# Kernel optimization log

Hardware: AMD Instinct MI355X
Metric: run time of the kernel (lower is better)

Reference implementation:

```python
import jax, jax.numpy as jnp
import numpy as np

B, S, D, H = 4, 2048, 1024, 4
HD = D // H


def setup_inputs() -> dict:
    key = jax.random.key(0)
    ks = jax.random.split(key, 6)
    s = 0.02  # init scale for projection weights
    return {
        "hidden_states": jax.random.normal(ks[0], (B, S, D), jnp.float32),
        "Wq": jax.random.normal(ks[1], (D, D), jnp.float32) * s,
        "Wk": jax.random.normal(ks[2], (D, D), jnp.float32) * s,
        "Wv": jax.random.normal(ks[3], (D, D), jnp.float32) * s,
        "Wo": jax.random.normal(ks[4], (D, D), jnp.float32) * s,
        "bo": jnp.zeros((D,), jnp.float32),
        "betas": jax.random.normal(ks[5], (1, H, 1, 1), jnp.float32),
        "mem": jnp.zeros((H, HD, HD), jnp.float32),
        "z": jnp.zeros((H, HD, 1), jnp.float32),
    }


def reference(hidden_states, Wq, Wk, Wv, Wo, bo, betas, mem, z):
    b, s, d = hidden_states.shape
    h = betas.shape[1]
    hd = d // h

    def split(x):  # [b,s,d] -> [b,h,s,hd]
        return x.reshape(b, s, h, hd).transpose(0, 2, 1, 3)

    q = split(hidden_states @ Wq.T)
    k = split(hidden_states @ Wk.T)
    v = split(hidden_states @ Wv.T)

    # standard causal attention (note: no 1/sqrt(d) scaling, faithful to source)
    aw = jnp.einsum('bhqd,bhkd->bhqk', q, k)
    causal = jnp.tril(jnp.ones((s, s), bool))
    aw = jnp.where(causal, aw, jnp.finfo(aw.dtype).min)
    p = jax.nn.softmax(aw, axis=-1)
    attn = jnp.einsum('bhqk,bhkd->bhqd', p, v)

    # linear-attention memory read
    sq = jax.nn.elu(q) + 1.0
    sk = jax.nn.elu(k) + 1.0
    A_mem = jnp.einsum('bhsd,hde->bhse', sq, mem) / (
        jnp.einsum('bhsd,hdo->bhso', sq, z) + 1e-6)

    # sigmoid-gated blend
    g = jax.nn.sigmoid(betas)
    out = g * A_mem + (1.0 - g) * attn

    # memory / z state update (delta rule), averaged over batch
    delta = jnp.einsum('bhsd,hde->bhse', sk, mem) / (
        jnp.einsum('bhsd,hdo->bhso', sk, z) + 1e-6)
    mem_new = mem + jnp.einsum('bhsd,bhse->hde', sk, v - delta) / b
    z_new = z + jnp.mean(jnp.sum(sk, axis=2), axis=0)[:, :, None]

    # merge heads + output projection
    out = out.transpose(0, 2, 1, 3).reshape(b, s, d)
    out = out @ Wo.T + bo
    return (out, mem_new, z_new)
```

## Files before the change

kernel.cpp:

```cpp
#include <hip/hip_runtime.h>

#define Bsz 4
#define Ssz 2048
#define Dsz 1024
#define Hsz 4
#define HDsz 256
#define Msz 8192

typedef unsigned short u16;
typedef __attribute__((ext_vector_type(8))) short bf16x8;
typedef __attribute__((ext_vector_type(4))) float f32x4;

__device__ __forceinline__ u16 f2b(float f) {
  unsigned u = __float_as_uint(f);
  return (u16)((u + 0x7FFFu + ((u >> 16) & 1u)) >> 16);
}
__device__ __forceinline__ unsigned pk2(float a, float b) {
  return (unsigned)f2b(a) | ((unsigned)f2b(b) << 16);
}

typedef const unsigned int __attribute__((address_space(1)))* gcp;
typedef unsigned int __attribute__((address_space(3)))* lcp;
__device__ __forceinline__ void gld16(const u16* g, u16* l) {
  __builtin_amdgcn_global_load_lds((gcp)g, (lcp)l, 16, 0, 0);
}

__global__ __launch_bounds__(256) void cvt_bf16(const float4* __restrict__ in,
                                                u16* __restrict__ outp) {
  size_t i = (size_t)blockIdx.x * 256 + threadIdx.x;
  float4 v = in[i];
  uint2 r; r.x = pk2(v.x, v.y); r.y = pk2(v.z, v.w);
  *(uint2*)(outp + i * 4) = r;
}

__global__ __launch_bounds__(256) void gemm_lds(const u16* __restrict__ A16,
                                                const u16* __restrict__ Wb,
                                                const float* __restrict__ bias,
                                                float* __restrict__ C32,
                                                u16* __restrict__ Cbf) {
  __shared__ u16 sA[128 * 32];
  __shared__ u16 sB[128 * 32];
  const int tid = threadIdx.x;
  const int lane = tid & 63, quad = lane >> 4, l15 = lane & 15;
  const int w = tid >> 6;
  const int mw = (w >> 1) * 64, nw = (w & 1) * 64;
  const int m0 = blockIdx.y * 128, n0 = blockIdx.x * 128;
  const int r0 = tid >> 2, seg = (tid & 3) * 8;
  const u16* ga0 = A16 + (size_t)(m0 + r0) * Dsz + seg;
  const u16* gb0 = Wb + (size_t)(n0 + r0) * Dsz + seg;
  u16* lA0 = sA + w * 512;
  u16* lA1 = sA + 2048 + w * 512;
  u16* lB0 = sB + w * 512;
  u16* lB1 = sB + 2048 + w * 512;
  f32x4 acc[4][4] = {};
  for (int k0 = 0; k0 < Dsz; k0 += 32) {
    __syncthreads();
    gld16(ga0 + k0, lA0);
    gld16(ga0 + (size_t)64 * Dsz + k0, lA1);
    gld16(gb0 + k0, lB0);
    gld16(gb0 + (size_t)64 * Dsz + k0, lB1);
    __syncthreads();
    bf16x8 af[4], bfr[4];
#pragma unroll
    for (int i = 0; i < 4; ++i) {
      af[i] = *(const bf16x8*)&sA[(mw + i * 16 + l15) * 32 + quad * 8];
      bfr[i] = *(const bf16x8*)&sB[(nw + i * 16 + l15) * 32 + quad * 8];
    }
#pragma unroll
    for (int i = 0; i < 4; ++i)
#pragma unroll
      for (int j = 0; j < 4; ++j)
        acc[i][j] = __builtin_amdgcn_mfma_f32_16x16x32_bf16(af[i], bfr[j], acc[i][j], 0, 0, 0);
  }
#pragma unroll
  for (int j = 0; j < 4; ++j) {
    const int n = n0 + nw + j * 16 + l15;
    const float bv = bias ? bias[n] : 0.f;
#pragma unroll
    for (int i = 0; i < 4; ++i) {
#pragma unroll
      for (int r = 0; r < 4; ++r) {
        const int m = m0 + mw + i * 16 + quad * 4 + r;
        const float val = acc[i][j][r] + bv;
        const size_t idx = (size_t)m * Dsz + n;
        if (C32) C32[idx] = val;
        if (Cbf) Cbf[idx] = f2b(val);
      }
    }
  }
}

__global__ __launch_bounds__(256) void transpose_v(const float* __restrict__ V,
                                                   u16* __restrict__ Vt) {
  __shared__ u16 tile[32 * 36];
  const int t = threadIdx.x;
  const int s0 = blockIdx.x * 32, e0 = blockIdx.y * 32, bh = blockIdx.z;
  const int b = bh >> 2, h = bh & 3;
  {
    const int s_l = t >> 3, e8 = (t & 7) * 4;
    float4 v = *(const float4*)(V + ((size_t)(b * Ssz) + s0 + s_l) * Dsz + h * HDsz + e0 + e8);
    uint2 r; r.x = pk2(v.x, v.y); r.y = pk2(v.z, v.w);
    *(uint2*)&tile[s_l * 36 + e8] = r;
  }
  __syncthreads();
  {
    const int e_l = t >> 3, s4 = (t & 7) * 4;
    u16 a = tile[(s4 + 0) * 36 + e_l], b2 = tile[(s4 + 1) * 36 + e_l];
    u16 c = tile[(s4 + 2) * 36 + e_l], d = tile[(s4 + 3) * 36 + e_l];
    uint2 r; r.x = (unsigned)a | ((unsigned)b2 << 16);
    r.y = (unsigned)c | ((unsigned)d << 16);
    *(uint2*)(Vt + ((size_t)bh * HDsz + e0 + e_l) * Ssz + s0 + s4) = r;
  }
}

__global__ __launch_bounds__(256) void attn_mfma(const u16* __restrict__ Qg,
                                                 const u16* __restrict__ Kg,
                                                 const u16* __restrict__ Vtg,
                                                 float* __restrict__ At,
                                                 float* __restrict__ Pb,
                                                 float* __restrict__ mlb) {
  static const unsigned char tab[52] = {
      (unsigned char)(31|0x80), (unsigned char)(31|0xC0),
      (unsigned char)(30|0x80), (unsigned char)(30|0xC0),
      (unsigned char)(29|0x80), (unsigned char)(29|0xC0),
      (unsigned char)(28|0x80), (unsigned char)(28|0xC0),
      (unsigned char)(27|0x80), (unsigned char)(27|0xC0),
      (unsigned char)(26|0x80), (unsigned char)(26|0xC0),
      (unsigned char)(25|0x80), (unsigned char)(25|0xC0),
      (unsigned char)(24|0x80), (unsigned char)(24|0xC0),
      (unsigned char)(23|0x80), (unsigned char)(23|0xC0),
      11,
      (unsigned char)(22|0x80), (unsigned char)(22|0xC0),
      (unsigned char)(21|0x80), (unsigned char)(21|0xC0),
      10,
      (unsigned char)(20|0x80), (unsigned char)(20|0xC0),
      (unsigned char)(19|0x80), (unsigned char)(19|0xC0),
      9,
      (unsigned char)(18|0x80), (unsigned char)(18|0xC0),
      (unsigned char)(17|0x80), (unsigned char)(17|0xC0),
      8,
      (unsigned char)(16|0x80), (unsigned char)(16|0xC0),
      (unsigned char)(15|0x80), (unsigned char)(15|0xC0),
      7,
      (unsigned char)(14|0x80), (unsigned char)(14|0xC0),
      (unsigned char)(13|0x80), (unsigned char)(13|0xC0),
      6,
      (unsigned char)(12|0x80), (unsigned char)(12|0xC0),
      5, 4, 3, 2, 1, 0};
  const int e = tab[blockIdx.x];
  const int qt = e & 63, cc = (e >> 6) & 1;
  const bool split = (e >> 7) != 0;
  const int bh = blockIdx.y, b = bh >> 2, h = bh & 3;
  const int tid = threadIdx.x, w = tid >> 6, lane = tid & 63;
  const int quad = lane >> 4, l15 = lane & 15;
  __shared__ u16 sK[2][32 * 256];
  __shared__ u16 sV[2][256 * 32];
  const int q0w = qt * 64 + w * 16;
  bf16x8 qf[8];
  {
    const u16* qp = Qg + ((size_t)(b * Ssz) + q0w + l15) * Dsz + h * HDsz + quad * 8;
#pragma unroll
    for (int dd = 0; dd < 8; ++dd) qf[dd] = *(const bf16x8*)(qp + dd * 32);
  }
  f32x4 o[16] = {};
  float m_old = -1e30f, l = 0.f;
  const int nkt = 2 * qt + 2, half = qt + 1;
  const int kt_lo = (split && cc) ? half : 0;
  const int kt_hi = (split && !cc) ? half : nkt;
  const u16* kstage = Kg + ((size_t)(b * Ssz) + (tid >> 5)) * Dsz + h * HDsz
                      + (((tid & 31) ^ ((tid >> 5) & 7)) << 3);
  const u16* vstage = Vtg + ((size_t)bh * HDsz + (tid >> 2)) * Ssz
                      + (((tid & 3) ^ ((tid >> 3) & 3)) << 3);
  int bufc = 0;
  {
    const u16* kp = kstage + (size_t)(kt_lo * 32) * Dsz;
    const u16* vp = vstage + kt_lo * 32;
#pragma unroll
    for (int i = 0; i < 4; ++i) {
      gld16(kp + (size_t)i * 8 * Dsz, &sK[0][w * 512 + i * 2048]);
      gld16(vp + (size_t)i * 64 * Ssz, &sV[0][w * 512 + i * 2048]);
    }
  }
  for (int kt = kt_lo; kt < kt_hi; ++kt) {
    const int j0 = kt * 32;
    __syncthreads();
    if (kt + 1 < kt_hi) {
      const u16* kp = kstage + (size_t)((kt + 1) * 32) * Dsz;
      const u16* vp = vstage + (kt + 1) * 32;
      const int bn = bufc ^ 1;
#pragma unroll
      for (int i = 0; i < 4; ++i) {
        gld16(kp + (size_t)i * 8 * Dsz, &sK[bn][w * 512 + i * 2048]);
        gld16(vp + (size_t)i * 64 * Ssz, &sV[bn][w * 512 + i * 2048]);
      }
    }
    f32x4 s0v = {}, s1v = {};
    __builtin_amdgcn_s_setprio(1);
#pragma unroll
    for (int dd = 0; dd < 8; ++dd) {
      const int c0 = ((dd * 4 + quad) ^ (l15 & 7)) << 3;
      bf16x8 a0 = *(const bf16x8*)&sK[bufc][l15 * 256 + c0];
      bf16x8 a1 = *(const bf16x8*)&sK[bufc][(16 + l15) * 256 + c0];
      s0v = __builtin_amdgcn_mfma_f32_16x16x32_bf16(a0, qf[dd], s0v, 0, 0, 0);
      s1v = __builtin_amdgcn_mfma_f32_16x16x32_bf16(a1, qf[dd], s1v, 0, 0, 0);
    }
    __builtin_amdgcn_s_setprio(0);
    const int qg = q0w + l15;
    float p[8];
#pragma unroll
    for (int r = 0; r < 4; ++r) {
      const int kg = j0 + quad * 4 + r;
      p[r] = (kg <= qg) ? s0v[r] : -1e30f;
      p[4 + r] = (kg + 16 <= qg) ? s1v[r] : -1e30f;
    }
    float mt = p[0];
#pragma unroll
    for (int i = 1; i < 8; ++i) mt = fmaxf(mt, p[i]);
    mt = fmaxf(mt, __shfl_xor(mt, 16));
    mt = fmaxf(mt, __shfl_xor(mt, 32));
    const float m_new = fmaxf(m_old, mt);
    const float alpha = __expf(m_old - m_new);
    float ts = 0.f;
#pragma unroll
    for (int i = 0; i < 8; ++i) { p[i] = __expf(p[i] - m_new); ts += p[i]; }
    ts += __shfl_xor(ts, 16);
    ts += __shfl_xor(ts, 32);
    l = l * alpha + ts;
    m_old = m_new;
    if (!__all(alpha == 1.0f)) {
      const float a0_ = __shfl(alpha, (lane & 48) | (quad * 4 + 0));
      const float a1_ = __shfl(alpha, (lane & 48) | (quad * 4 + 1));
      const float a2_ = __shfl(alpha, (lane & 48) | (quad * 4 + 2));
      const float a3_ = __shfl(alpha, (lane & 48) | (quad * 4 + 3));
#pragma unroll
      for (int ds = 0; ds < 16; ++ds) {
        o[ds][0] *= a0_; o[ds][1] *= a1_; o[ds][2] *= a2_; o[ds][3] *= a3_;
      }
    }
    float xx[8];
#pragma unroll
    for (int i = 0; i < 8; ++i) xx[i] = __shfl_xor(p[i], 16);
    const bool qe = (quad & 1) == 0;
    float Alo[8], Ahi[8];
#pragma unroll
    for (int i = 0; i < 4; ++i) {
      Alo[i] = qe ? p[i] : xx[i];
      Alo[4 + i] = qe ? xx[i] : p[i];
      Ahi[i] = qe ? p[4 + i] : xx[4 + i];
      Ahi[4 + i] = qe ? xx[4 + i] : p[4 + i];
    }
    float zz[8];
    const bool sendlo = (quad & 1) != 0;
#pragma unroll
    for (int i = 0; i < 8; ++i) zz[i] = __shfl_xor(sendlo ? Alo[i] : Ahi[i], 32);
    float fin[8];
#pragma unroll
    for (int i = 0; i < 8; ++i)
      fin[i] = (quad == 0) ? Alo[i] : (quad == 3) ? Ahi[i] : zz[i];
    uint4 pkv;
    pkv.x = pk2(fin[0], fin[1]); pkv.y = pk2(fin[2], fin[3]);
    pkv.z = pk2(fin[4], fin[5]); pkv.w = pk2(fin[6], fin[7]);
    bf16x8 pf = *(bf16x8*)&pkv;
    const int vc0 = (quad ^ ((l15 >> 1) & 3)) << 3;
    __builtin_amdgcn_s_setprio(1);
#pragma unroll
    for (int ds = 0; ds < 16; ++ds) {
      bf16x8 bv = *(const bf16x8*)&sV[bufc][(ds * 16 + l15) * 32 + vc0];
      o[ds] = __builtin_amdgcn_mfma_f32_16x16x32_bf16(pf, bv, o[ds], 0, 0, 0);
    }
    __builtin_amdgcn_s_setprio(0);
    bufc ^= 1;
  }
  if (!split) {
    float lr[4];
#pragma unroll
    for (int r = 0; r < 4; ++r) lr[r] = 1.f / __shfl(l, (lane & 48) | (quad * 4 + r));
    float* ob = At + ((size_t)bh * Ssz + q0w + quad * 4) * HDsz + l15;
#pragma unroll
    for (int r = 0; r < 4; ++r)
#pragma unroll
      for (int ds = 0; ds < 16; ++ds)
        ob[(size_t)r * HDsz + ds * 16] = o[ds][r] * lr[r];
  } else {
    float* dst;
    if (cc == 0)
      dst = At + ((size_t)bh * Ssz + q0w + quad * 4) * HDsz + l15;
    else
      dst = Pb + ((size_t)((bh * 20 + (qt - 12)) * 64) + w * 16 + quad * 4) * HDsz + l15;
#pragma unroll
    for (int r = 0; r < 4; ++r)
#pragma unroll
      for (int ds = 0; ds < 16; ++ds)
        dst[(size_t)r * HDsz + ds * 16] = o[ds][r];
    if (lane < 16) {
      const int idx = (bh * 20 + (qt - 12)) * 64 + w * 16 + l15;
      mlb[cc * 40960 + idx] = m_old;
      mlb[cc * 40960 + 20480 + idx] = l;
    }
  }
}

__global__ __launch_bounds__(256) void attn_merge(float* __restrict__ At,
                                                  const float* __restrict__ Pb,
                                                  const float* __restrict__ mlb) {
  const int qx = blockIdx.x, bh = blockIdx.y;
  const int t = threadIdx.x;
  const int slot = (bh * 20 + qx) * 64;
  float4* abase = (float4*)(At + ((size_t)bh * Ssz + (12 + qx) * 64) * HDsz);
  const float4* pbase = (const float4*)(Pb + (size_t)slot * HDsz);
#pragma unroll
  for (int i = 0; i < 16; ++i) {
    const int f = i * 256 + t;
    const int qr = f >> 6;
    const int idx = slot + qr;
    const float m0 = mlb[idx], l0 = mlb[20480 + idx];
    const float m1 = mlb[40960 + idx], l1 = mlb[61440 + idx];
    const float mm = fmaxf(m0, m1);
    const float w0 = __expf(m0 - mm), w1 = __expf(m1 - mm);
    const float inv = 1.f / (l0 * w0 + l1 * w1);
    float4 av = abase[f];
    float4 pv = pbase[f];
    float4 ov;
    ov.x = (av.x * w0 + pv.x * w1) * inv;
    ov.y = (av.y * w0 + pv.y * w1) * inv;
    ov.z = (av.z * w0 + pv.z * w1) * inv;
    ov.w = (av.w * w0 + pv.w * w1) * inv;
    abase[f] = ov;
  }
}

__global__ __launch_bounds__(256) void eludens(float* __restrict__ Qb,
                                               float* __restrict__ Kb,
                                               const float* __restrict__ z,
                                               float* __restrict__ dq,
                                               float* __restrict__ dk) {
  const int wid = threadIdx.x >> 6, lane = threadIdx.x & 63;
  const int r = blockIdx.x * 4 + wid;
  const int b = r >> 13, h = (r >> 11) & 3, s = r & 2047;
  const size_t base = ((size_t)(b * Ssz + s)) * Dsz + h * HDsz + lane * 4;
  float4 z4 = *(const float4*)(z + h * HDsz + lane * 4);
  float4 q = *(float4*)(Qb + base);
  q.x = q.x > 0.f ? q.x + 1.f : __expf(q.x);
  q.y = q.y > 0.f ? q.y + 1.f : __expf(q.y);
  q.z = q.z > 0.f ? q.z + 1.f : __expf(q.z);
  q.w = q.w > 0.f ? q.w + 1.f : __expf(q.w);
  *(float4*)(Qb + base) = q;
  float4 k = *(float4*)(Kb + base);
  k.x = k.x > 0.f ? k.x + 1.f : __expf(k.x);
  k.y = k.y > 0.f ? k.y + 1.f : __expf(k.y);
  k.z = k.z > 0.f ? k.z + 1.f : __expf(k.z);
  k.w = k.w > 0.f ? k.w + 1.f : __expf(k.w);
  *(float4*)(Kb + base) = k;
  float pq = q.x * z4.x + q.y * z4.y + q.z * z4.z + q.w * z4.w;
  float pk = k.x * z4.x + k.y * z4.y + k.z * z4.z + k.w * z4.w;
#pragma unroll
  for (int off = 32; off; off >>= 1) {
    pq += __shfl_down(pq, off);
    pk += __shfl_down(pk, off);
  }
  if (lane == 0) { dq[r] = pq; dk[r] = pk; }
}

__global__ __launch_bounds__(256) void memread_mfma(const float* __restrict__ Asrc,
                                                    const float* __restrict__ mem,
                                                    const float* __restrict__ dens,
                                                    const float* __restrict__ betas,
                                                    const float* __restrict__ At,
                                                    float* __restrict__ Vio,
                                                    u16* __restrict__ bfout, int mode) {
  const int h = blockIdx.z;
  const int tid = threadIdx.x, lane = tid & 63, w = tid >> 6;
  const int quad = lane >> 4, l15 = lane & 15;
  const int mw = (w >> 1) * 64, ew = (w & 1) * 64;
  const int m0 = blockIdx.y * 128, e0t = blockIdx.x * 128;
  __shared__ u16 sA[128 * 40];
  __shared__ u16 sB[128 * 40];
  const int srow = tid >> 1, sseg = (tid & 1) * 16;
  const int k4 = (tid & 7) * 4, e4 = (tid >> 3) * 4;
  f32x4 acc[4][4] = {};
  for (int k0 = 0; k0 < HDsz; k0 += 32) {
    __syncthreads();
    {
      const float* ap = Asrc + (size_t)(m0 + srow) * Dsz + h * HDsz + k0 + sseg;
      float4 f0 = *(const float4*)ap, f1 = *(const float4*)(ap + 4);
      float4 f2 = *(const float4*)(ap + 8), f3 = *(const float4*)(ap + 12);
      uint4 u0, u1;
      u0.x = pk2(f0.x, f0.y); u0.y = pk2(f0.z, f0.w);
      u0.z = pk2(f1.x, f1.y); u0.w = pk2(f1.z, f1.w);
      u1.x = pk2(f2.x, f2.y); u1.y = pk2(f2.z, f2.w);
      u1.z = pk2(f3.x, f3.y); u1.w = pk2(f3.z, f3.w);
      u16* dst = &sA[srow * 40 + sseg];
      *(uint4*)dst = u0; *(uint4*)(dst + 8) = u1;
    }
    {
      const float* bp = mem + (size_t)h * 65536 + (size_t)(k0 + k4) * HDsz + e0t + e4;
      float4 r0 = *(const float4*)bp;
      float4 r1 = *(const float4*)(bp + HDsz);
      float4 r2 = *(const float4*)(bp + 2 * HDsz);
      float4 r3 = *(const float4*)(bp + 3 * HDsz);
      const float* rr[4] = {(const float*)&r0, (const float*)&r1,
                            (const float*)&r2, (const float*)&r3};
#pragma unroll
      for (int c = 0; c < 4; ++c) {
        uint2 u;
        u.x = pk2(rr[0][c], rr[1][c]);
        u.y = pk2(rr[2][c], rr[3][c]);
        *(uint2*)&sB[(e4 + c) * 40 + k4] = u;
      }
    }
    __syncthreads();
    bf16x8 af[4], bfr[4];
#pragma unroll
    for (int i = 0; i < 4; ++i) {
      af[i] = *(const bf16x8*)&sA[(mw + i * 16 + l15) * 40 + quad * 8];
      bfr[i] = *(const bf16x8*)&sB[(ew + i * 16 + l15) * 40 + quad * 8];
    }
#pragma unroll
    for (int i = 0; i < 4; ++i)
#pragma unroll
      for (int j = 0; j < 4; ++j)
        acc[i][j] = __builtin_amdgcn_mfma_f32_16x16x32_bf16(af[i], bfr[j], acc[i][j], 0, 0, 0);
  }
  const float g = 1.f / (1.f + __expf(-betas[h]));
#pragma unroll
  for (int i = 0; i < 4; ++i) {
#pragma unroll
    for (int r = 0; r < 4; ++r) {
      const int m = m0 + mw + i * 16 + quad * 4 + r;
      const int b = m >> 11, s = m & 2047;
      const int rowidx = ((b << 2) + h) * Ssz + s;
      const float inv = 1.f / (dens[rowidx] + 1e-6f);
#pragma unroll
      for (int j = 0; j < 4; ++j) {
        const int e = e0t + ew + j * 16 + l15;
        const float av = acc[i][j][r] * inv;
        if (mode == 0) {
          const float a = At[(size_t)rowidx * HDsz + e];
          bfout[(size_t)m * Dsz + h * HDsz + e] = f2b(g * av + (1.f - g) * a);
        } else {
          float* p = Vio + (size_t)m * Dsz + h * HDsz + e;
          *p = *p - av;
        }
      }
    }
  }
}

__global__ __launch_bounds__(256) void mem_update_mfma(const float* __restrict__ SK,
                                                       const float* __restrict__ W,
                                                       float* __restrict__ P) {
  const int de = blockIdx.x;
  const int d0 = (de >> 1) * 128, e0 = (de & 1) * 128;
  const int h = blockIdx.y, chunk = blockIdx.z;
  const int m0 = chunk * 512;
  const int tid = threadIdx.x, lane = tid & 63, w = tid >> 6;
  const int quad = lane >> 4, l15 = lane & 15;
  const int dw = (w >> 1) * 64, ew = (w & 1) * 64;
  __shared__ u16 sA[128 * 40];
  __shared__ u16 sB[128 * 40];
  const int m4 = (tid & 7) * 4;
  const int c4 = (tid >> 3) * 4;
  f32x4 acc[4][4] = {};
  for (int mt = 0; mt < 512; mt += 32) {
    __syncthreads();
    const float* ka = SK + (size_t)(m0 + mt + m4) * Dsz + h * HDsz + d0 + c4;
    const float* wa = W + (size_t)(m0 + mt + m4) * Dsz + h * HDsz + e0 + c4;
    float4 a0 = *(const float4*)ka;
    float4 a1 = *(const float4*)(ka + Dsz);
    float4 a2 = *(const float4*)(ka + 2 * Dsz);
    float4 a3 = *(const float4*)(ka + 3 * Dsz);
    float4 b0 = *(const float4*)wa;
    float4 b1 = *(const float4*)(wa + Dsz);
    float4 b2 = *(const float4*)(wa + 2 * Dsz);
    float4 b3 = *(const float4*)(wa + 3 * Dsz);
    const float* aa[4] = {(const float*)&a0, (const float*)&a1,
                          (const float*)&a2, (const float*)&a3};
    const float* bb[4] = {(const float*)&b0, (const float*)&b1,
                          (const float*)&b2, (const float*)&b3};
#pragma unroll
    for (int c = 0; c < 4; ++c) {
      uint2 ua, ub2;
      ua.x = pk2(aa[0][c], aa[1][c]); ua.y = pk2(aa[2][c], aa[3][c]);
      ub2.x = pk2(bb[0][c], bb[1][c]); ub2.y = pk2(bb[2][c], bb[3][c]);
      *(uint2*)&sA[(c4 + c) * 40 + m4] = ua;
      *(uint2*)&sB[(c4 + c) * 40 + m4] = ub2;
    }
    __syncthreads();
    bf16x8 af[4], bfr[4];
#pragma unroll
    for (int i = 0; i < 4; ++i) {
      af[i] = *(const bf16x8*)&sA[(dw + i * 16 + l15) * 40 + quad * 8];
      bfr[i] = *(const bf16x8*)&sB[(ew + i * 16 + l15) * 40 + quad * 8];
    }
#pragma unroll
    for (int i = 0; i < 4; ++i)
#pragma unroll
      for (int j = 0; j < 4; ++j)
        acc[i][j] = __builtin_amdgcn_mfma_f32_16x16x32_bf16(af[i], bfr[j], acc[i][j], 0, 0, 0);
  }
  float* Pp = P + ((size_t)(h * 16 + chunk)) * 65536;
#pragma unroll
  for (int i = 0; i < 4; ++i)
#pragma unroll
    for (int r = 0; r < 4; ++r) {
      const int d = d0 + dw + i * 16 + quad * 4 + r;
#pragma unroll
      for (int j = 0; j < 4; ++j) {
        const int e = e0 + ew + j * 16 + l15;
        Pp[(size_t)d * HDsz + e] = acc[i][j][r];
      }
    }
}

__global__ __launch_bounds__(256) void mem_reduce(const float4* __restrict__ P,
                                                  const float4* __restrict__ mem,
                                                  float4* __restrict__ outmem) {
  const int gid = blockIdx.x * 256 + threadIdx.x;
  const int h = gid >> 14, off = gid & 16383;
  float sx = 0.f, sy = 0.f, sz = 0.f, sw = 0.f;
#pragma unroll 4
  for (int c = 0; c < 16; ++c) {
    float4 v = P[((size_t)(h * 16 + c) << 14) + off];
    sx += v.x; sy += v.y; sz += v.z; sw += v.w;
  }
  float4 m = mem[gid];
  float4 o;
  o.x = m.x + 0.25f * sx; o.y = m.y + 0.25f * sy;
  o.z = m.z + 0.25f * sz; o.w = m.w + 0.25f * sw;
  outmem[gid] = o;
}

__global__ __launch_bounds__(256) void z_update(const float* __restrict__ SK,
                                                const float* __restrict__ z_in,
                                                float* __restrict__ z_out) {
  __shared__ float4 red[256];
  const int h = blockIdx.x >> 7, chunk = blockIdx.x & 127;
  const int wid = threadIdx.x >> 6, lane = threadIdx.x & 63;
  const int m0 = chunk * 64;
  float4 s = {0.f, 0.f, 0.f, 0.f};
#pragma unroll
  for (int i = 0; i < 16; ++i) {
    const int row = m0 + i * 4 + wid;
    float4 v = *(const float4*)(SK + (size_t)row * Dsz + h * HDsz + lane * 4);
    s.x += v.x; s.y += v.y; s.z += v.z; s.w += v.w;
  }
  red[wid * 64 + lane] = s;
  __syncthreads();
  if (wid == 0) {
    float4 a = red[lane], b = red[64 + lane], c = red[128 + lane], d = red[192 + lane];
    a.x = (a.x + b.x + c.x + d.x) * 0.25f;
    a.y = (a.y + b.y + c.y + d.y) * 0.25f;
    a.z = (a.z + b.z + c.z + d.z) * 0.25f;
    a.w = (a.w + b.w + c.w + d.w) * 0.25f;
    if (chunk == 0) {
      const float4 z4 = *(const float4*)(z_in + h * HDsz + lane * 4);
      a.x += z4.x; a.y += z4.y; a.z += z4.z; a.w += z4.w;
    }
    float* zp = z_out + h * HDsz + lane * 4;
    atomicAdd(zp + 0, a.x);
    atomicAdd(zp + 1, a.y);
    atomicAdd(zp + 2, a.z);
    atomicAdd(zp + 3, a.w);
  }
}

extern "C" void kernel_launch(void* const* d_in, const int* in_sizes, int n_in,
                              void* d_out, int out_size, void* d_ws, size_t ws_size,
                              hipStream_t stream) {
  (void)in_sizes; (void)n_in; (void)out_size; (void)ws_size;
  const float* Hs = (const float*)d_in[0];
  const float* Wq = (const float*)d_in[1];
  const float* Wk = (const float*)d_in[2];
  const float* Wv = (const float*)d_in[3];
  const float* Wo = (const float*)d_in[4];
  const float* bo = (const float*)d_in[5];
  const float* betas = (const float*)d_in[6];
  const float* mem = (const float*)d_in[7];
  const float* z = (const float*)d_in[8];

  float* ws = (float*)d_ws;
  float* Qb = ws;
  float* Kb = ws + 8388608;
  float* Vb = ws + 16777216;
  float* At = ws + 25165824;
  float* dq = ws + 33554432;
  float* dk = ws + 33587200;
  float* mlb = ws + 33619968;
  u16* ub = (u16*)(ws + 33701888);
  u16* Wqb = ub;
  u16* Wkb = ub + 1048576;
  u16* Wvb = ub + 2097152;
  u16* Wob = ub + 3145728;
  u16* Qbf = ub + 4194304;
  u16* Kbf = ub + 12582912;
  u16* Vt = ub + 20971520;
  u16* Hsb = Vt;
  float* P = (float*)Vt;
  float* Pb = (float*)d_out;

  float* out = (float*)d_out;
  float* outmem = out + (size_t)Msz * Dsz;
  float* outz = outmem + Hsz * HDsz * HDsz;

  hipMemsetAsync(outz, 0, (size_t)(Hsz * HDsz) * sizeof(float), stream);

  cvt_bf16<<<1024, 256, 0, stream>>>((const float4*)Wq, Wqb);
  cvt_bf16<<<1024, 256, 0, stream>>>((const float4*)Wk, Wkb);
  cvt_bf16<<<1024, 256, 0, stream>>>((const float4*)Wv, Wvb);
  cvt_bf16<<<1024, 256, 0, stream>>>((const float4*)Wo, Wob);
  cvt_bf16<<<8192, 256, 0, stream>>>((const float4*)Hs, Hsb);

  dim3 gg(8, 64);
  gemm_lds<<<gg, 256, 0, stream>>>(Hsb, Wqb, nullptr, Qb, Qbf);
  gemm_lds<<<gg, 256, 0, stream>>>(Hsb, Wkb, nullptr, Kb, Kbf);
  gemm_lds<<<gg, 256, 0, stream>>>(Hsb, Wvb, nullptr, Vb, nullptr);

  transpose_v<<<dim3(64, 8, 16), 256, 0, stream>>>(Vb, Vt);
  attn_mfma<<<dim3(52, 16), 256, 0, stream>>>(Qbf, Kbf, Vt, At, Pb, mlb);
  attn_merge<<<dim3(20, 16), 256, 0, stream>>>(At, Pb, mlb);

  eludens<<<8192, 256, 0, stream>>>(Qb, Kb, z, dq, dk);

  memread_mfma<<<dim3(2, 64, 4), 256, 0, stream>>>(Qb, mem, dq, betas, At, nullptr, Qbf, 0);
  memread_mfma<<<dim3(2, 64, 4), 256, 0, stream>>>(Kb, mem, dk, betas, nullptr, Vb, nullptr, 1);

  mem_update_mfma<<<dim3(4, 4, 16), 256, 0, stream>>>(Kb, Vb, P);
  mem_reduce<<<256, 256, 0, stream>>>((const float4*)P, (const float4*)mem, (float4*)outmem);
  z_update<<<512, 256, 0, stream>>>(Kb, z, outz);

  gemm_lds<<<gg, 256, 0, stream>>>(Qbf, Wob, bo, out, nullptr);
}
```

Measured before the change: 554.5 us.

## Single-buffer V tile, split QK accumulation chains, and swizzle GEMM block order

The attention kernel now keeps a single V buffer in shared memory. V for the current tile is loaded at the start of each iteration and waited on with an extra barrier before the PV MFMAs, which reduces LDS use and may raise occupancy. The QK^T dot product is split into two independent accumulator chains to shorten MFMA dependency latency, and the s_setprio hints are removed. The GEMM remaps block indices so that neighbouring blocks share tiles for better L2 reuse. In exchange, the V load is no longer prefetched a full iteration ahead and each iteration pays an extra barrier.

Measured after the change: 523.7 us. 1.06x faster.

```diff
diff --git a/kernel.cpp b/kernel.cpp
--- a/kernel.cpp
+++ b/kernel.cpp
@@ -44,7 +44,9 @@
   const int lane = tid & 63, quad = lane >> 4, l15 = lane & 15;
   const int w = tid >> 6;
   const int mw = (w >> 1) * 64, nw = (w & 1) * 64;
-  const int m0 = blockIdx.y * 128, n0 = blockIdx.x * 128;
+  const int bid = blockIdx.y * 8 + blockIdx.x;
+  const int nb = (bid & 7) * 64 + (bid >> 3);
+  const int m0 = (nb >> 3) * 128, n0 = (nb & 7) * 128;
   const int r0 = tid >> 2, seg = (tid & 3) * 8;
   const u16* ga0 = A16 + (size_t)(m0 + r0) * Dsz + seg;
   const u16* gb0 = Wb + (size_t)(n0 + r0) * Dsz + seg;
@@ -154,7 +156,7 @@
   const int tid = threadIdx.x, w = tid >> 6, lane = tid & 63;
   const int quad = lane >> 4, l15 = lane & 15;
   __shared__ u16 sK[2][32 * 256];
-  __shared__ u16 sV[2][256 * 32];
+  __shared__ u16 sV[256 * 32];
   const int q0w = qt * 64 + w * 16;
   bf16x8 qf[8];
   {
@@ -174,37 +176,41 @@
   int bufc = 0;
   {
     const u16* kp = kstage + (size_t)(kt_lo * 32) * Dsz;
-    const u16* vp = vstage + kt_lo * 32;
-#pragma unroll
-    for (int i = 0; i < 4; ++i) {
+#pragma unroll
+    for (int i = 0; i < 4; ++i)
       gld16(kp + (size_t)i * 8 * Dsz, &sK[0][w * 512 + i * 2048]);
-      gld16(vp + (size_t)i * 64 * Ssz, &sV[0][w * 512 + i * 2048]);
-    }
   }
   for (int kt = kt_lo; kt < kt_hi; ++kt) {
     const int j0 = kt * 32;
     __syncthreads();
+    {
+      const u16* vp = vstage + kt * 32;
+#pragma unroll
+      for (int i = 0; i < 4; ++i)
+        gld16(vp + (size_t)i * 64 * Ssz, &sV[w * 512 + i * 2048]);
+    }
     if (kt + 1 < kt_hi) {
       const u16* kp = kstage + (size_t)((kt + 1) * 32) * Dsz;
-      const u16* vp = vstage + (kt + 1) * 32;
       const int bn = bufc ^ 1;
 #pragma unroll
-      for (int i = 0; i < 4; ++i) {
+      for (int i = 0; i < 4; ++i)
         gld16(kp + (size_t)i * 8 * Dsz, &sK[bn][w * 512 + i * 2048]);
-        gld16(vp + (size_t)i * 64 * Ssz, &sV[bn][w * 512 + i * 2048]);
-      }
-    }
-    f32x4 s0v = {}, s1v = {};
-    __builtin_amdgcn_s_setprio(1);
-#pragma unroll
-    for (int dd = 0; dd < 8; ++dd) {
+    }
+    f32x4 s0a = {}, s0b = {}, s1a = {}, s1b = {};
+#pragma unroll
+    for (int dd = 0; dd < 4; ++dd) {
       const int c0 = ((dd * 4 + quad) ^ (l15 & 7)) << 3;
+      const int c1 = (((dd + 4) * 4 + quad) ^ (l15 & 7)) << 3;
       bf16x8 a0 = *(const bf16x8*)&sK[bufc][l15 * 256 + c0];
       bf16x8 a1 = *(const bf16x8*)&sK[bufc][(16 + l15) * 256 + c0];
-      s0v = __builtin_amdgcn_mfma_f32_16x16x32_bf16(a0, qf[dd], s0v, 0, 0, 0);
-      s1v = __builtin_amdgcn_mfma_f32_16x16x32_bf16(a1, qf[dd], s1v, 0, 0, 0);
-    }
-    __builtin_amdgcn_s_setprio(0);
+      bf16x8 b0 = *(const bf16x8*)&sK[bufc][l15 * 256 + c1];
+      bf16x8 b1 = *(const bf16x8*)&sK[bufc][(16 + l15) * 256 + c1];
+      s0a = __builtin_amdgcn_mfma_f32_16x16x32_bf16(a0, qf[dd], s0a, 0, 0, 0);
+      s1a = __builtin_amdgcn_mfma_f32_16x16x32_bf16(a1, qf[dd], s1a, 0, 0, 0);
+      s0b = __builtin_amdgcn_mfma_f32_16x16x32_bf16(b0, qf[dd + 4], s0b, 0, 0, 0);
+      s1b = __builtin_amdgcn_mfma_f32_16x16x32_bf16(b1, qf[dd + 4], s1b, 0, 0, 0);
+    }
+    f32x4 s0v = s0a + s0b, s1v = s1a + s1b;
     const int qg = q0w + l15;
     float p[8];
 #pragma unroll
@@ -262,13 +268,12 @@
     pkv.z = pk2(fin[4], fin[5]); pkv.w = pk2(fin[6], fin[7]);
     bf16x8 pf = *(bf16x8*)&pkv;
     const int vc0 = (quad ^ ((l15 >> 1) & 3)) << 3;
-    __builtin_amdgcn_s_setprio(1);
+    __syncthreads();
 #pragma unroll
     for (int ds = 0; ds < 16; ++ds) {
-      bf16x8 bv = *(const bf16x8*)&sV[bufc][(ds * 16 + l15) * 32 + vc0];
+      bf16x8 bv = *(const bf16x8*)&sV[(ds * 16 + l15) * 32 + vc0];
       o[ds] = __builtin_amdgcn_mfma_f32_16x16x32_bf16(pf, bv, o[ds], 0, 0, 0);
     }
-    __builtin_amdgcn_s_setprio(0);
     bufc ^= 1;
   }
   if (!split) {
```
